# Performance work log

Measured on AMD Instinct MI355X. Metric: run time of the kernel, lower is better.

The kernel has to match this reference:

```python
import jax, jax.numpy as jnp
import numpy as np

HEAD = 8
C = 32  # dhead
SCALE = 0.17677669529663687  # 1/sqrt(32)


def setup_inputs() -> dict:
    key = jax.random.key(0)
    k1, k2, k3, k4 = jax.random.split(key, 4)
    N, S, R, M = 1, 256, 384, 256
    msa_repr = jax.random.normal(k1, (N, S, R, M), dtype=jnp.float32)
    # 0.02 init scale keeps softmax logits / sigmoid pre-activations in a sane range
    gate_proj = jax.random.normal(k2, (M, M), dtype=jnp.float32) * 0.02
    qkv_proj = jax.random.normal(k3, (M, 3 * M), dtype=jnp.float32) * 0.02
    out_proj = jax.random.normal(k4, (M, M), dtype=jnp.float32) * 0.02
    return {"msa_repr": msa_repr, "gate_proj": gate_proj, "qkv_proj": qkv_proj, "out_proj": out_proj}


def reference(msa_repr, gate_proj, qkv_proj, out_proj):
    # col_attn: permute [N,S,R,M] -> [N,R,S,M]; attention runs over the residue axis S
    x = jnp.transpose(msa_repr, (0, 2, 1, 3))  # [N,R,S,M]
    N, R, S, M = x.shape
    gate = jax.nn.sigmoid(x @ gate_proj).reshape(N, R, S, HEAD, C)
    q, k, v = jnp.split(x @ qkv_proj, 3, axis=-1)  # each [N,R,S,M]
    q = q.reshape(N, R, S, HEAD, C)
    k = k.reshape(N, R, S, HEAD, C)
    v = v.reshape(N, R, S, HEAD, C)
    sim = jnp.einsum('nrihc,nrjhc->nrhij', q, k) * jnp.float32(SCALE)  # [N,R,H,S,S]
    attn = jax.nn.softmax(sim, axis=-1)
    out = jnp.einsum('nrhij,nrjhc->nrihc', attn, v) * gate  # [N,R,S,H,C]
    out = out.reshape(N, R, S, HEAD * C) @ out_proj  # [N,R,S,M]
    return jnp.transpose(out, (0, 2, 1, 3))  # back to [N,S,R,M]
```

## Files before the change

### kernel.cpp

```cpp
#include <hip/hip_runtime.h>
#include <hip/hip_bf16.h>

#define R_DIM 384
#define S_DIM 256
#define M_DIM 256

typedef __attribute__((ext_vector_type(4))) float  f32x4;
typedef __attribute__((ext_vector_type(4))) float  fvec4;
typedef __attribute__((ext_vector_type(8))) short  short8;
typedef __attribute__((ext_vector_type(4))) short  short4v;

__device__ __forceinline__ short f2bf(float f) {
    __hip_bfloat16 h = __float2bfloat16(f);
    return __builtin_bit_cast(short, h);
}
__device__ __forceinline__ float bf2f(short s) {
    return __bfloat162float(__builtin_bit_cast(__hip_bfloat16, s));
}

__device__ __forceinline__ void gload_lds16(const void* gsrc, void* ldst) {
    __builtin_amdgcn_global_load_lds(
        (const __attribute__((address_space(1))) unsigned int*)gsrc,
        (__attribute__((address_space(3))) unsigned int*)ldst, 16, 0, 0);
}

#define QSCALE (0.17677669529663687f * 1.4426950408889634f)

__global__ __launch_bounds__(256) void k_prep(
    const float* __restrict__ gp, const float* __restrict__ qkvp,
    const float* __restrict__ op, short* __restrict__ Wt1,
    short* __restrict__ Wot)
{
    __shared__ float tile[64][65];
    const int tx = threadIdx.x & 63, ty = threadIdx.x >> 6;
    const int k0 = blockIdx.x * 64;
    const int j0 = blockIdx.y * 64;
    const float* src; int ld, cb;
    if (j0 < 256)       { src = gp;   ld = 256; cb = j0; }
    else if (j0 < 1024) { src = qkvp; ld = 768; cb = j0 - 256; }
    else                { src = op;   ld = 256; cb = j0 - 1024; }
    for (int q = 0; q < 16; ++q) {
        const int kk = q * 4 + ty;
        tile[kk][tx] = src[(k0 + kk) * ld + cb + tx];
    }
    __syncthreads();
    for (int q = 0; q < 16; ++q) {
        const int jj = q * 4 + ty;
        const int jglob = j0 + jj;
        const float scl = (jglob >= 256 && jglob < 512) ? QSCALE : 1.0f;
        const float val = tile[tx][jj] * scl;
        if (jglob < 1024) Wt1[jglob * 256 + k0 + tx] = f2bf(val);
        else              Wot[(jglob - 1024) * 256 + k0 + tx] = f2bf(val);
    }
}

__global__ __launch_bounds__(256, 3) void k_qkvgate(
    const float* __restrict__ msa, const short* __restrict__ Wt1,
    short* __restrict__ gate, short* __restrict__ qb,
    short* __restrict__ kb, short* __restrict__ vb)
{
    __shared__ __align__(16) char Al[64 * 512];
    __shared__ __align__(16) short Bl[2][128 * 32];
    const int tid = threadIdx.x;
    const int l = tid & 63, w = tid >> 6;
    const int wr = w >> 1, wc = w & 1;
    const int rowBase = blockIdx.x * 64;

    {
        const int arow0 = tid >> 6;
        const int col4  = (tid & 63) * 4;
        const int slot  = (tid & 63) >> 1;
        const int sub   = (tid & 63) & 1;
        for (int ii = 0; ii < 16; ++ii) {
            const int a_r = ii * 4 + arow0;
            const int i = rowBase + a_r;
            const int rr = i >> 8, ss = i & 255;
            fvec4 vv = *(const fvec4*)(msa + ((ss * R_DIM + rr) << 8) + col4);
            short4v b4;
            b4.x = f2bf(vv.x); b4.y = f2bf(vv.y);
            b4.z = f2bf(vv.z); b4.w = f2bf(vv.w);
            *(short4v*)(Al + a_r * 512 + ((slot ^ (a_r & 7)) << 4) + sub * 8) = b4;
        }
    }

    auto stageB = [&](int tt, short* buf) {
        const int cb = (tt >> 3) * 128, k0 = (tt & 7) * 32;
        #pragma unroll
        for (int r = 0; r < 2; ++r) {
            const int L = r * 256 + w * 64 + l;
            const int row = L >> 2, psl = L & 3;
            const int gsl = psl ^ ((row >> 1) & 3);
            gload_lds16(Wt1 + (cb + row) * 256 + k0 + gsl * 8,
                        buf + (r * 256 + w * 64) * 8);
        }
    };

    stageB(0, (short*)Bl[0]);
    __syncthreads();

    short8 af[8][2];
    #pragma unroll
    for (int kc = 0; kc < 8; ++kc) {
        const int aslot = kc * 4 + (l >> 4);
        #pragma unroll
        for (int it = 0; it < 2; ++it) {
            const int row = wr * 32 + it * 16 + (l & 15);
            af[kc][it] = *(const short8*)(Al + row * 512 + ((aslot ^ (row & 7)) << 4));
        }
    }

    short* AlT = (short*)Al;
    const int rr_blk = rowBase >> 8;
    const int ssBase = rowBase & 255;

    f32x4 acc[2][4] = {};
    for (int ct = 0; ct < 8; ++ct) {
        #pragma unroll
        for (int kc = 0; kc < 8; ++kc) {
            const int t = ct * 8 + kc;
            if (t + 1 < 64) stageB(t + 1, (short*)Bl[(kc + 1) & 1]);

            const short* Bb = (const short*)Bl[kc & 1];
            short8 bfr[4];
            #pragma unroll
            for (int jt = 0; jt < 4; ++jt) {
                const int row = wc * 64 + jt * 16 + (l & 15);
                const int psl = (l >> 4) ^ ((row >> 1) & 3);
                bfr[jt] = *(const short8*)(Bb + row * 32 + psl * 8);
            }
            #pragma unroll
            for (int it = 0; it < 2; ++it)
                #pragma unroll
                for (int jt = 0; jt < 4; ++jt)
                    acc[it][jt] = __builtin_amdgcn_mfma_f32_16x16x32_bf16(
                        af[kc][it], bfr[jt], acc[it][jt], 0, 0, 0);

            __syncthreads();
        }
        const int colBase = ct * 128;
        const int sel = ct >> 1;
        if (sel < 3) {
            short* dst = (sel == 0) ? gate : (sel == 1) ? qb : kb;
            #pragma unroll
            for (int it = 0; it < 2; ++it) {
                const int base_i = rowBase + wr * 32 + it * 16 + ((l >> 4) << 2);
                #pragma unroll
                for (int reg = 0; reg < 4; ++reg) {
                    const int i = base_i + reg;
                    const int rr = i >> 8, ss = i & 255;
                    #pragma unroll
                    for (int jt = 0; jt < 4; ++jt) {
                        const int jg = colBase + wc * 64 + jt * 16 + (l & 15);
                        const int jj = jg & 255;
                        const int h = jj >> 5, c = jj & 31;
                        float vv = acc[it][jt][reg];
                        if (sel == 0) vv = 1.0f / (1.0f + __builtin_amdgcn_exp2f(-vv * 1.4426950408889634f));
                        dst[(((rr << 3) + h) * 256 + ss) * 32 + c] = f2bf(vv);
                    }
                }
            }
        } else {
            const int jjBase = (colBase & 255);
            #pragma unroll
            for (int it = 0; it < 2; ++it) {
                const int ssL0 = wr * 32 + it * 16 + ((l >> 4) << 2);
                #pragma unroll
                for (int reg = 0; reg < 4; ++reg) {
                    #pragma unroll
                    for (int jt = 0; jt < 4; ++jt) {
                        const int jjL = wc * 64 + jt * 16 + (l & 15);
                        AlT[jjL * 72 + ssL0 + reg] = f2bf(acc[it][jt][reg]);
                    }
                }
            }
            __syncthreads();
            #pragma unroll
            for (int q = 0; q < 4; ++q) {
                const int cid = q * 256 + tid;
                const int jjL = cid >> 3, sc = cid & 7;
                short8 vv8 = *(const short8*)(&AlT[jjL * 72 + sc * 8]);
                const int jj = jjBase + jjL;
                const int h = jj >> 5, c = jj & 31;
                const int pp = (rr_blk << 3) + h;
                *(short8*)(vb + (pp << 13) + (c << 8) + ssBase + sc * 8) = vv8;
            }
        }
        #pragma unroll
        for (int it = 0; it < 2; ++it)
            #pragma unroll
            for (int jt = 0; jt < 4; ++jt)
                acc[it][jt] = (f32x4){0.f, 0.f, 0.f, 0.f};
    }
}

__global__ __launch_bounds__(256) void k_attn(
    short* qo, const short* __restrict__ kb, const short* __restrict__ vb,
    const short* __restrict__ gate)
{
    __shared__ __align__(16) short Pl[4 * 32 * 68];
    const int tid = threadIdx.x;
    const int l = tid & 63, w = tid >> 6;
    const int p = blockIdx.x;
    short* qg = qo + p * 8192;
    const short* kg = kb + p * 8192;
    const short* vg = vb + p * 8192;
    const short* gg = gate + p * 8192;
    const int c0 = (l >> 4) * 8;

    short8 qf[4];
    #pragma unroll
    for (int it = 0; it < 4; ++it) {
        const int s = w * 64 + it * 16 + (l & 15);
        qf[it] = *(const short8*)(qg + s * 32 + c0);
    }

    f32x4 oacc[4][2] = {};
    f32x4 ssum[4] = {};
    short8 bones;
    #pragma unroll
    for (int e = 0; e < 8; ++e) bones[e] = (short)0x3F80;
    short* Pw = &Pl[w * (32 * 68)];

    for (int ch = 0; ch < 4; ++ch) {
        const int j0 = ch * 64;
        f32x4 sacc[4][4] = {};
        short8 kf[4];
        #pragma unroll
        for (int jt = 0; jt < 4; ++jt) {
            const int row = j0 + jt * 16 + (l & 15);
            kf[jt] = *(const short8*)(kg + row * 32 + c0);
        }
        #pragma unroll
        for (int it = 0; it < 4; ++it)
            #pragma unroll
            for (int jt = 0; jt < 4; ++jt)
                sacc[it][jt] = __builtin_amdgcn_mfma_f32_16x16x32_bf16(
                    qf[it], kf[jt], sacc[it][jt], 0, 0, 0);

        short8 vfa[2][2];
        #pragma unroll
        for (int kk = 0; kk < 2; ++kk)
            #pragma unroll
            for (int cti = 0; cti < 2; ++cti)
                vfa[kk][cti] = *(const short8*)(
                    vg + (cti * 16 + (l & 15)) * 256 + j0 + kk * 32 + (l >> 4) * 8);

        #pragma unroll
        for (int ih = 0; ih < 2; ++ih) {
            #pragma unroll
            for (int itl = 0; itl < 2; ++itl) {
                const int it = ih * 2 + itl;
                #pragma unroll
                for (int reg = 0; reg < 4; ++reg) {
                    const int rowl = itl * 16 + ((l >> 4) << 2) + reg;
                    #pragma unroll
                    for (int jt = 0; jt < 4; ++jt)
                        Pw[rowl * 68 + jt * 16 + (l & 15)] =
                            f2bf(__builtin_amdgcn_exp2f(sacc[it][jt][reg]));
                }
            }
            #pragma unroll
            for (int kk = 0; kk < 2; ++kk) {
                const int koff = kk * 32 + (l >> 4) * 8;
                short8 pf[2];
                #pragma unroll
                for (int itl = 0; itl < 2; ++itl)
                    pf[itl] = *(const short8*)(&Pw[(itl * 16 + (l & 15)) * 68 + koff]);
                #pragma unroll
                for (int itl = 0; itl < 2; ++itl) {
                    const int it = ih * 2 + itl;
                    #pragma unroll
                    for (int cti = 0; cti < 2; ++cti)
                        oacc[it][cti] = __builtin_amdgcn_mfma_f32_16x16x32_bf16(
                            pf[itl], vfa[kk][cti], oacc[it][cti], 0, 0, 0);
                    ssum[it] = __builtin_amdgcn_mfma_f32_16x16x32_bf16(
                        pf[itl], bones, ssum[it], 0, 0, 0);
                }
            }
        }
    }
    #pragma unroll
    for (int it = 0; it < 4; ++it) {
        #pragma unroll
        for (int reg = 0; reg < 4; ++reg) {
            const float inv = 1.0f / ssum[it][reg];
            const int s = w * 64 + it * 16 + ((l >> 4) << 2) + reg;
            #pragma unroll
            for (int cti = 0; cti < 2; ++cti) {
                const int c = cti * 16 + (l & 15);
                const float gv = bf2f(gg[s * 32 + c]);
                qg[s * 32 + c] = f2bf(oacc[it][cti][reg] * inv * gv);
            }
        }
    }
}

__global__ __launch_bounds__(256, 4) void k_out(
    const short* __restrict__ ao, const short* __restrict__ Wot,
    float* __restrict__ out)
{
    __shared__ __align__(16) short Bl[2][128 * 32];
    const int tid = threadIdx.x;
    const int l = tid & 63, w = tid >> 6;
    const int wr = w >> 1, wc = w & 1;
    const int rowBase = blockIdx.y * 128;
    const int colBase = blockIdx.x * 128;

    auto stageB = [&](int kc, short* buf) {
        const int k0 = kc * 32;
        #pragma unroll
        for (int r = 0; r < 2; ++r) {
            const int L = r * 256 + w * 64 + l;
            const int row = L >> 2, psl = L & 3;
            const int gsl = psl ^ ((row >> 1) & 3);
            gload_lds16(Wot + (colBase + row) * 256 + k0 + gsl * 8,
                        buf + (r * 256 + w * 64) * 8);
        }
    };

    stageB(0, (short*)Bl[0]);
    __syncthreads();

    f32x4 acc[4][4] = {};
    #pragma unroll
    for (int kc = 0; kc < 8; ++kc) {
        if (kc + 1 < 8) stageB(kc + 1, (short*)Bl[(kc + 1) & 1]);

        short8 af[4];
        #pragma unroll
        for (int it = 0; it < 4; ++it) {
            const int i = rowBase + wr * 64 + it * 16 + (l & 15);
            const int rr = i >> 8, ss = i & 255;
            af[it] = *(const short8*)(ao + (((rr << 3) + kc) * 256 + ss) * 32 + (l >> 4) * 8);
        }
        const short* Bb = (const short*)Bl[kc & 1];
        short8 bfr[4];
        #pragma unroll
        for (int jt = 0; jt < 4; ++jt) {
            const int row = wc * 64 + jt * 16 + (l & 15);
            const int psl = (l >> 4) ^ ((row >> 1) & 3);
            bfr[jt] = *(const short8*)(Bb + row * 32 + psl * 8);
        }
        #pragma unroll
        for (int it = 0; it < 4; ++it)
            #pragma unroll
            for (int jt = 0; jt < 4; ++jt)
                acc[it][jt] = __builtin_amdgcn_mfma_f32_16x16x32_bf16(
                    af[it], bfr[jt], acc[it][jt], 0, 0, 0);

        __syncthreads();
    }
    #pragma unroll
    for (int it = 0; it < 4; ++it) {
        const int base_i = rowBase + wr * 64 + it * 16 + ((l >> 4) << 2);
        #pragma unroll
        for (int reg = 0; reg < 4; ++reg) {
            const int i = base_i + reg;
            const int rr = i >> 8, ss = i & 255;
            #pragma unroll
            for (int jt = 0; jt < 4; ++jt) {
                const int m = colBase + wc * 64 + jt * 16 + (l & 15);
                out[((ss * R_DIM + rr) << 8) + m] = acc[it][jt][reg];
            }
        }
    }
}

extern "C" void kernel_launch(void* const* d_in, const int* in_sizes, int n_in,
                              void* d_out, int out_size, void* d_ws, size_t ws_size,
                              hipStream_t stream) {
    const float* msa  = (const float*)d_in[0];
    const float* gp   = (const float*)d_in[1];
    const float* qkvp = (const float*)d_in[2];
    const float* op   = (const float*)d_in[3];
    float* out = (float*)d_out;
    char* ws = (char*)d_ws;

    const size_t SZ = 50331648;
    short* Wt1  = (short*)ws;
    short* Wot  = (short*)(ws + 524288);
    short* gate = (short*)(ws + 655360);
    short* qb   = (short*)(ws + 655360 + 1 * SZ);
    short* kb   = (short*)(ws + 655360 + 2 * SZ);
    short* vb   = (short*)(ws + 655360 + 3 * SZ);

    k_prep<<<dim3(4, 20), 256, 0, stream>>>(gp, qkvp, op, Wt1, Wot);
    k_qkvgate<<<dim3(1536), 256, 0, stream>>>(msa, Wt1, gate, qb, kb, vb);
    k_attn<<<dim3(3072), 256, 0, stream>>>(qb, kb, vb, gate);
    k_out<<<dim3(2, 768), 256, 0, stream>>>(qb, Wot, out);
}
```

Baseline: 222.0 us.

## Keep attention probabilities in registers by computing transposed scores

The attention kernel now computes S^T = K·Q^T per 16-key tile, so the MFMA output layout matches the A-operand layout of a 16x16x16 bf16 MFMA. The exponentiated probabilities are packed straight into registers and fed to the PV and row-sum MFMAs, removing the LDS round trip and the shared buffer. In exchange it uses the smaller-K MFMA instruction (more issues for the same work) and narrower V loads.

Result: no change. 220.3 us (median of 2 runs) (-0.7%).

```diff
diff --git a/kernel.cpp b/kernel.cpp
--- a/kernel.cpp
+++ b/kernel.cpp
@@ -9,6 +9,7 @@
 typedef __attribute__((ext_vector_type(4))) float  fvec4;
 typedef __attribute__((ext_vector_type(8))) short  short8;
 typedef __attribute__((ext_vector_type(4))) short  short4v;
+typedef __attribute__((ext_vector_type(2))) int    i32x2;
 
 __device__ __forceinline__ short f2bf(float f) {
     __hip_bfloat16 h = __float2bfloat16(f);
@@ -17,6 +18,20 @@
 __device__ __forceinline__ float bf2f(short s) {
     return __bfloat162float(__builtin_bit_cast(__hip_bfloat16, s));
 }
+
+#if __has_builtin(__builtin_amdgcn_mfma_f32_16x16x16bf16_1k)
+__device__ __forceinline__ f32x4 mfma16(short4v a, short4v b, f32x4 c) {
+    return __builtin_amdgcn_mfma_f32_16x16x16bf16_1k(a, b, c, 0, 0, 0);
+}
+#else
+__device__ __forceinline__ f32x4 mfma16(short4v a, short4v b, f32x4 c) {
+    f32x4 d;
+    asm volatile("v_mfma_f32_16x16x16_bf16 %0, %1, %2, %3\n\t"
+                 "s_nop 7\n\ts_nop 7"
+                 : "=&v"(d) : "v"(a), "v"(b), "v"(c));
+    return d;
+}
+#endif
 
 __device__ __forceinline__ void gload_lds16(const void* gsrc, void* ldst) {
     __builtin_amdgcn_global_load_lds(
@@ -197,7 +212,6 @@
     short* qo, const short* __restrict__ kb, const short* __restrict__ vb,
     const short* __restrict__ gate)
 {
-    __shared__ __align__(16) short Pl[4 * 32 * 68];
     const int tid = threadIdx.x;
     const int l = tid & 63, w = tid >> 6;
     const int p = blockIdx.x;
@@ -205,77 +219,60 @@
     const short* kg = kb + p * 8192;
     const short* vg = vb + p * 8192;
     const short* gg = gate + p * 8192;
-    const int c0 = (l >> 4) * 8;
+    const int r = l & 15, g = l >> 4;
+    const int c0 = g * 8;
 
     short8 qf[4];
     #pragma unroll
     for (int it = 0; it < 4; ++it) {
-        const int s = w * 64 + it * 16 + (l & 15);
+        const int s = w * 64 + it * 16 + r;
         qf[it] = *(const short8*)(qg + s * 32 + c0);
     }
 
     f32x4 oacc[4][2] = {};
     f32x4 ssum[4] = {};
-    short8 bones;
-    #pragma unroll
-    for (int e = 0; e < 8; ++e) bones[e] = (short)0x3F80;
-    short* Pw = &Pl[w * (32 * 68)];
+    short4v ones4;
+    ones4.x = (short)0x3F80; ones4.y = (short)0x3F80;
+    ones4.z = (short)0x3F80; ones4.w = (short)0x3F80;
 
     for (int ch = 0; ch < 4; ++ch) {
         const int j0 = ch * 64;
-        f32x4 sacc[4][4] = {};
         short8 kf[4];
         #pragma unroll
         for (int jt = 0; jt < 4; ++jt) {
-            const int row = j0 + jt * 16 + (l & 15);
+            const int row = j0 + jt * 16 + r;
             kf[jt] = *(const short8*)(kg + row * 32 + c0);
         }
         #pragma unroll
-        for (int it = 0; it < 4; ++it)
-            #pragma unroll
-            for (int jt = 0; jt < 4; ++jt)
-                sacc[it][jt] = __builtin_amdgcn_mfma_f32_16x16x32_bf16(
-                    qf[it], kf[jt], sacc[it][jt], 0, 0, 0);
-
-        short8 vfa[2][2];
-        #pragma unroll
-        for (int kk = 0; kk < 2; ++kk)
+        for (int jt = 0; jt < 4; ++jt) {
+            f32x4 st[4];
+            #pragma unroll
+            for (int it = 0; it < 4; ++it)
+                st[it] = __builtin_amdgcn_mfma_f32_16x16x32_bf16(
+                    kf[jt], qf[it], (f32x4){0.f, 0.f, 0.f, 0.f}, 0, 0, 0);
+            short4v pf[4];
+            #pragma unroll
+            for (int it = 0; it < 4; ++it) {
+                const unsigned u0 =
+                    (unsigned)(unsigned short)f2bf(__builtin_amdgcn_exp2f(st[it][0])) |
+                    ((unsigned)(unsigned short)f2bf(__builtin_amdgcn_exp2f(st[it][1])) << 16);
+                const unsigned u1 =
+                    (unsigned)(unsigned short)f2bf(__builtin_amdgcn_exp2f(st[it][2])) |
+                    ((unsigned)(unsigned short)f2bf(__builtin_amdgcn_exp2f(st[it][3])) << 16);
+                i32x2 t; t.x = (int)u0; t.y = (int)u1;
+                pf[it] = __builtin_bit_cast(short4v, t);
+            }
+            short4v vf[2];
             #pragma unroll
             for (int cti = 0; cti < 2; ++cti)
-                vfa[kk][cti] = *(const short8*)(
-                    vg + (cti * 16 + (l & 15)) * 256 + j0 + kk * 32 + (l >> 4) * 8);
-
-        #pragma unroll
-        for (int ih = 0; ih < 2; ++ih) {
-            #pragma unroll
-            for (int itl = 0; itl < 2; ++itl) {
-                const int it = ih * 2 + itl;
+                vf[cti] = *(const short4v*)(
+                    vg + (cti * 16 + r) * 256 + j0 + jt * 16 + g * 4);
+            #pragma unroll
+            for (int it = 0; it < 4; ++it) {
                 #pragma unroll
-                for (int reg = 0; reg < 4; ++reg) {
-                    const int rowl = itl * 16 + ((l >> 4) << 2) + reg;
-                    #pragma unroll
-                    for (int jt = 0; jt < 4; ++jt)
-                        Pw[rowl * 68 + jt * 16 + (l & 15)] =
-                            f2bf(__builtin_amdgcn_exp2f(sacc[it][jt][reg]));
-                }
-            }
-            #pragma unroll
-            for (int kk = 0; kk < 2; ++kk) {
-                const int koff = kk * 32 + (l >> 4) * 8;
-                short8 pf[2];
-                #pragma unroll
-                for (int itl = 0; itl < 2; ++itl)
-                    pf[itl] = *(const short8*)(&Pw[(itl * 16 + (l & 15)) * 68 + koff]);
-                #pragma unroll
-                for (int itl = 0; itl < 2; ++itl) {
-                    const int it = ih * 2 + itl;
-                    #pragma unroll
-                    for (int cti = 0; cti < 2; ++cti)
-                        oacc[it][cti] = __builtin_amdgcn_mfma_f32_16x16x32_bf16(
-                            pf[itl], vfa[kk][cti], oacc[it][cti], 0, 0, 0);
-                    ssum[it] = __builtin_amdgcn_mfma_f32_16x16x32_bf16(
-                        pf[itl], bones, ssum[it], 0, 0, 0);
-                }
+                for (int cti = 0; cti < 2; ++cti)
+                    oacc[it][cti] = mfma16(pf[it], vf[cti], oacc[it][cti]);
+                ssum[it] = mfma16(pf[it], ones4, ssum[it]);
             }
         }
     }
@@ -284,10 +281,10 @@
         #pragma unroll
         for (int reg = 0; reg < 4; ++reg) {
             const float inv = 1.0f / ssum[it][reg];
-            const int s = w * 64 + it * 16 + ((l >> 4) << 2) + reg;
+            const int s = w * 64 + it * 16 + (g << 2) + reg;
             #pragma unroll
             for (int cti = 0; cti < 2; ++cti) {
-                const int c = cti * 16 + (l & 15);
+                const int c = cti * 16 + r;
                 const float gv = bf2f(gg[s * 32 + c]);
                 qg[s * 32 + c] = f2bf(oacc[it][cti][reg] * inv * gv);
             }
```
